# Kernel optimization log

Measured on AMD Instinct MI355X. Metric: run time of the kernel, lower is better.

## Reference

```python
import jax, jax.numpy as jnp
import numpy as np

DT = 0.01
OMEGA_MAX = 100.0


def setup_inputs() -> dict:
    key = jax.random.key(0)
    ks = jax.random.split(key, 7)
    B, T, D, M = 4, 4096, 1024, 64
    N = 2 * M
    u = jax.random.normal(ks[0], (B, T, D), dtype=jnp.float32)
    W_omega = jax.random.normal(ks[1], (M, D), dtype=jnp.float32) * 0.02
    b_omega = jnp.ones((M,), dtype=jnp.float32)
    W_zeta = jax.random.normal(ks[2], (M, D), dtype=jnp.float32) * 0.02
    b_zeta = jnp.zeros((M,), dtype=jnp.float32)
    W_B = jax.random.normal(ks[3], (N, D), dtype=jnp.float32) * (0.1 / np.sqrt(D))
    b_B = jnp.zeros((N,), dtype=jnp.float32)
    C = jax.random.normal(ks[4], (D, N), dtype=jnp.float32) * 0.01
    D_mat = jax.random.normal(ks[5], (D, D), dtype=jnp.float32) * 0.01
    return dict(u=u, W_omega=W_omega, b_omega=b_omega, W_zeta=W_zeta,
                b_zeta=b_zeta, W_B=W_B, b_B=b_B, C=C, D_mat=D_mat)


def reference(u, W_omega, b_omega, W_zeta, b_zeta, W_B, b_B, C, D_mat):
    B, T, D = u.shape
    M = W_omega.shape[0]
    # Hoist all per-step linear projections into batched GEMMs (same math).
    omega = jax.nn.softplus(jnp.einsum('btd,md->btm', u, W_omega) + b_omega)
    omega = jnp.clip(omega, 1e-4, OMEGA_MAX)                      # (B,T,M)
    zeta = jax.nn.sigmoid(jnp.einsum('btd,md->btm', u, W_zeta) + b_zeta)
    A = omega * omega                                             # (B,T,M)
    S = 1.0 / (1.0 + (DT * DT) * A)                               # (B,T,M)
    d = 1.0 - zeta                                                # (B,T,M)
    F = jnp.einsum('btd,nd->btn', u, W_B) + b_B                   # (B,T,2M)

    def step(x, inp):
        A_t, S_t, d_t, F_t = inp                                  # (B,M)x3, (B,2M)
        z = x[:, :M]
        y = x[:, M:]
        z_new = d_t * (S_t * z - DT * A_t * S_t * y)
        y_new = d_t * (DT * S_t * z + S_t * y)
        x_new = jnp.concatenate([z_new, y_new], axis=-1) + F_t
        return x_new, x_new

    x0 = jnp.zeros((B, 2 * M), dtype=u.dtype)
    tm = lambda a: jnp.swapaxes(a, 0, 1)  # to time-major for scan
    _, xs = jax.lax.scan(step, x0, (tm(A), tm(S), tm(d), tm(F)))
    xs = jnp.swapaxes(xs, 0, 1)                                   # (B,T,2M)
    # Output projection: y_t = x_t C^T + u_t D^T
    y = jnp.einsum('btn,dn->btd', xs, C) + jnp.einsum('bte,de->btd', u, D_mat)
    return y
```

## Files before the change

### kernel.cpp

```cpp
#include <hip/hip_runtime.h>
#include <hip/hip_bf16.h>
#include <math.h>

#define DTC 0.01f

typedef __attribute__((ext_vector_type(8))) short short8;
typedef __attribute__((ext_vector_type(4))) float f32x4;
typedef unsigned short bf16raw;

__device__ __forceinline__ bf16raw f2bf(float f){
  union { unsigned u; float f; } v; v.f = f;
  unsigned r = v.u + 0x7FFF + ((v.u >> 16) & 1u);
  return (bf16raw)(r >> 16);
}

__device__ __forceinline__ short8 ld8f(const float* __restrict__ p){
  float4 a = *(const float4*)p;
  float4 b = *(const float4*)(p + 4);
  short8 r;
  r[0] = (short)f2bf(a.x); r[1] = (short)f2bf(a.y);
  r[2] = (short)f2bf(a.z); r[3] = (short)f2bf(a.w);
  r[4] = (short)f2bf(b.x); r[5] = (short)f2bf(b.y);
  r[6] = (short)f2bf(b.z); r[7] = (short)f2bf(b.w);
  return r;
}

template<int ITERS>
__device__ __forceinline__ void stage_async(const bf16raw* __restrict__ src, long ld,
                                            long row0, int k0, bf16raw* lds,
                                            int wave, int lane){
  int kchunk = (lane & 3) ^ ((lane >> 3) & 3);
#pragma unroll
  for (int i = 0; i < ITERS; ++i){
    int r0 = (wave*ITERS + i) * 16;
    long row = row0 + r0 + (lane >> 2);
    const bf16raw* gp = src + row*ld + k0 + kchunk*8;
    bf16raw* lp = lds + r0*32;
    __builtin_amdgcn_global_load_lds((const __attribute__((address_space(1))) void*)gp,
                                     (__attribute__((address_space(3))) void*)lp,
                                     16, 0, 0);
  }
}

template<int MI, int NI>
__device__ __forceinline__ void mma_tile(const bf16raw* Alds, const bf16raw* Blds,
                                         f32x4 acc[MI][NI], int wm, int wn, int quad, int t16){
  short8 af[MI], bfr[NI];
  int sw = (quad ^ ((t16 >> 1) & 3)) * 8;
#pragma unroll
  for (int mi = 0; mi < MI; ++mi)
    af[mi] = *(const short8*)(Alds + (wm*(MI*16) + mi*16 + t16)*32 + sw);
#pragma unroll
  for (int ni = 0; ni < NI; ++ni)
    bfr[ni] = *(const short8*)(Blds + (wn*(NI*16) + ni*16 + t16)*32 + sw);
#pragma unroll
  for (int mi = 0; mi < MI; ++mi)
#pragma unroll
    for (int ni = 0; ni < NI; ++ni)
      acc[mi][ni] = __builtin_amdgcn_mfma_f32_16x16x32_bf16(af[mi], bfr[ni], acc[mi][ni], 0, 0, 0);
}

extern "C" __global__ void k_prep(const float* __restrict__ u,
    const float* __restrict__ Wom, const float* __restrict__ Wze,
    const float* __restrict__ WB, const float* __restrict__ Cm,
    const float* __restrict__ Dm, bf16raw* __restrict__ u_bf,
    bf16raw* __restrict__ Wcat, bf16raw* __restrict__ C_bf,
    bf16raw* __restrict__ Dm_bf){
  long g = (long)blockIdx.x * 256 + threadIdx.x;
  const float* src; bf16raw* dst; long o;
  if      (g < 2097152){ src = u;   dst = u_bf;          o = g; }
  else if (g < 2105344){ src = Wom; dst = Wcat;          o = g - 2097152; }
  else if (g < 2113536){ src = Wze; dst = Wcat + 65536;  o = g - 2105344; }
  else if (g < 2129920){ src = WB;  dst = Wcat + 131072; o = g - 2113536; }
  else if (g < 2146304){ src = Cm;  dst = C_bf;          o = g - 2129920; }
  else                 { src = Dm;  dst = Dm_bf;         o = g - 2146304; }
  *(short8*)(dst + o*8) = ld8f(src + o*8);
}

extern "C" __global__ __launch_bounds__(256, 4) void k_gemm_p(
    const bf16raw* __restrict__ u_bf, const bf16raw* __restrict__ Wcat,
    float* __restrict__ P){
  __shared__ __align__(16) bf16raw Alds[3*64*32];
  __shared__ __align__(16) bf16raw Blds[3*64*32];
  int tid = threadIdx.x, wave = tid >> 6, lane = tid & 63;
  int quad = lane >> 4, t16 = lane & 15;
  int wm = wave >> 1, wn = wave & 1;
  int id  = blockIdx.y * gridDim.x + blockIdx.x;
  int sid = (id & 7) * 128 + (id >> 3);
  long row0 = (long)(sid >> 2) * 64;
  int  col0 = (sid & 3) * 64;
  f32x4 acc[2][2] = {};

  auto stage = [&](int kt, int buf){
    stage_async<1>(u_bf, 1024, row0, kt*32, Alds + buf*(64*32), wave, lane);
    stage_async<1>(Wcat, 1024, col0, kt*32, Blds + buf*(64*32), wave, lane);
  };

  stage(0, 0);
  stage(1, 1);
  int rd = 0;
  for (int s = 0; s < 30; ++s){
    asm volatile("s_waitcnt vmcnt(2)" ::: "memory");
    __builtin_amdgcn_s_barrier();
    __builtin_amdgcn_sched_barrier(0);
    int st = rd >= 1 ? rd - 1 : 2;
    stage(s + 2, st);
    __builtin_amdgcn_s_setprio(1);
    mma_tile<2,2>(Alds + rd*(64*32), Blds + rd*(64*32), acc, wm, wn, quad, t16);
    __builtin_amdgcn_s_setprio(0);
    rd = rd < 2 ? rd + 1 : 0;
  }
  asm volatile("s_waitcnt vmcnt(2)" ::: "memory");
  __builtin_amdgcn_s_barrier();
  __builtin_amdgcn_sched_barrier(0);
  mma_tile<2,2>(Alds + 0*(64*32), Blds + 0*(64*32), acc, wm, wn, quad, t16);
  asm volatile("s_waitcnt vmcnt(0)" ::: "memory");
  __builtin_amdgcn_s_barrier();
  __builtin_amdgcn_sched_barrier(0);
  mma_tile<2,2>(Alds + 1*(64*32), Blds + 1*(64*32), acc, wm, wn, quad, t16);
#pragma unroll
  for (int mi = 0; mi < 2; ++mi)
#pragma unroll
    for (int ni = 0; ni < 2; ++ni)
#pragma unroll
      for (int r = 0; r < 4; ++r){
        long grow = row0 + wm*32 + mi*16 + quad*4 + r;
        int  gcol = col0 + wn*32 + ni*16 + t16;
        P[grow*256 + gcol] = acc[mi][ni][r];
      }
}

extern "C" __global__ __launch_bounds__(256, 3) void k_gemm_out(
    const bf16raw* __restrict__ Xs, const bf16raw* __restrict__ u_bf,
    const bf16raw* __restrict__ C_bf, const bf16raw* __restrict__ Dm_bf,
    float* __restrict__ out){
  __shared__ __align__(16) bf16raw Alds[3*128*32];
  __shared__ __align__(16) bf16raw Blds[3*128*32];
  int tid = threadIdx.x, wave = tid >> 6, lane = tid & 63;
  int quad = lane >> 4, t16 = lane & 15;
  int wm = wave >> 1, wn = wave & 1;
  int id  = blockIdx.y * gridDim.x + blockIdx.x;
  int sid = (id & 7) * 128 + (id >> 3);
  long row0 = (long)(sid >> 3) * 128;
  int  col0 = (sid & 7) * 128;
  f32x4 acc[4][4] = {};

  auto stage = [&](int s, int buf){
    if (s < 4){
      stage_async<2>(Xs,   128, row0, s*32, Alds + buf*(128*32), wave, lane);
      stage_async<2>(C_bf, 128, col0, s*32, Blds + buf*(128*32), wave, lane);
    } else {
      stage_async<2>(u_bf,  1024, row0, (s-4)*32, Alds + buf*(128*32), wave, lane);
      stage_async<2>(Dm_bf, 1024, col0, (s-4)*32, Blds + buf*(128*32), wave, lane);
    }
  };

  stage(0, 0);
  stage(1, 1);
  int rd = 0;
  for (int s = 0; s < 34; ++s){
    asm volatile("s_waitcnt vmcnt(4)" ::: "memory");
    __builtin_amdgcn_s_barrier();
    __builtin_amdgcn_sched_barrier(0);
    int st = rd >= 1 ? rd - 1 : 2;
    stage(s + 2, st);
    __builtin_amdgcn_s_setprio(1);
    mma_tile<4,4>(Alds + rd*(128*32), Blds + rd*(128*32), acc, wm, wn, quad, t16);
    __builtin_amdgcn_s_setprio(0);
    rd = rd < 2 ? rd + 1 : 0;
  }
  asm volatile("s_waitcnt vmcnt(4)" ::: "memory");
  __builtin_amdgcn_s_barrier();
  __builtin_amdgcn_sched_barrier(0);
  mma_tile<4,4>(Alds + 1*(128*32), Blds + 1*(128*32), acc, wm, wn, quad, t16);
  asm volatile("s_waitcnt vmcnt(0)" ::: "memory");
  __builtin_amdgcn_s_barrier();
  __builtin_amdgcn_sched_barrier(0);
  mma_tile<4,4>(Alds + 2*(128*32), Blds + 2*(128*32), acc, wm, wn, quad, t16);
#pragma unroll
  for (int mi = 0; mi < 4; ++mi)
#pragma unroll
    for (int ni = 0; ni < 4; ++ni)
#pragma unroll
      for (int r = 0; r < 4; ++r){
        long grow = row0 + wm*64 + mi*16 + quad*4 + r;
        int  gcol = col0 + wn*64 + ni*16 + t16;
        out[grow*1024 + gcol] = acc[mi][ni][r];
      }
}

extern "C" __global__ __launch_bounds__(256) void k_scanA(
    const float* __restrict__ P, const float* __restrict__ b_om,
    const float* __restrict__ b_ze, const float* __restrict__ b_B,
    float4* __restrict__ CM, float2* __restrict__ CV){
  int tid = threadIdx.x, c = blockIdx.x;
  int b = tid >> 6, m = tid & 63;
  float bo = b_om[m], bz = b_ze[m], bb0 = b_B[m], bb1 = b_B[64 + m];
  const float* row = P + ((size_t)b*4096 + c*16) * 256;
  float m00=1.f, m01=0.f, m10=0.f, m11=0.f, vz=0.f, vy=0.f;
#pragma unroll 4
  for (int t = 0; t < 16; ++t){
    const float* r = row + t*256;
    float wo = r[m]       + bo;
    float wz = r[64 + m]  + bz;
    float fz = r[128 + m] + bb0;
    float fy = r[192 + m] + bb1;
    float sp = (wo > 20.f) ? wo : log1pf(expf(wo));
    float omega = fminf(fmaxf(sp, 1e-4f), 100.f);
    float A = omega * omega;
    float S = 1.f / (1.f + DTC*DTC*A);
    float zeta = 1.f / (1.f + expf(-wz));
    float p = (1.f - zeta) * S;
    float q = p * DTC * A;
    float nvz = p*vz - q*vy + fz;
    float nvy = DTC*p*vz + p*vy + fy;
    vz = nvz; vy = nvy;
    float n00 = p*m00 - q*m10;
    float n01 = p*m01 - q*m11;
    float n10 = DTC*p*m00 + p*m10;
    float n11 = DTC*p*m01 + p*m11;
    m00=n00; m01=n01; m10=n10; m11=n11;
  }
  CM[c*256 + tid] = make_float4(m00, m01, m10, m11);
  CV[c*256 + tid] = make_float2(vz, vy);
}

extern "C" __global__ __launch_bounds__(256) void k_scanC(
    const float* __restrict__ P, const float* __restrict__ b_om,
    const float* __restrict__ b_ze, const float* __restrict__ b_B,
    const float4* __restrict__ CM, const float2* __restrict__ CV,
    bf16raw* __restrict__ Xs){
  int tid = threadIdx.x, c = blockIdx.x;
  int b = tid >> 6, m = tid & 63;
  float xz = 0.f, xy = 0.f;
#pragma unroll 4
  for (int j = 0; j < c; ++j){
    float4 Mv = CM[j*256 + tid];
    float2 Vv = CV[j*256 + tid];
    float nz = Mv.x*xz + Mv.y*xy + Vv.x;
    float ny = Mv.z*xz + Mv.w*xy + Vv.y;
    xz = nz; xy = ny;
  }
  float bo = b_om[m], bz = b_ze[m], bb0 = b_B[m], bb1 = b_B[64 + m];
  const float* row = P + ((size_t)b*4096 + c*16) * 256;
  bf16raw* xp = Xs + ((size_t)b*4096 + c*16) * 128 + m;
#pragma unroll 4
  for (int t = 0; t < 16; ++t){
    const float* r = row + t*256;
    float wo = r[m]       + bo;
    float wz = r[64 + m]  + bz;
    float fz = r[128 + m] + bb0;
    float fy = r[192 + m] + bb1;
    float sp = (wo > 20.f) ? wo : log1pf(expf(wo));
    float omega = fminf(fmaxf(sp, 1e-4f), 100.f);
    float A = omega * omega;
    float S = 1.f / (1.f + DTC*DTC*A);
    float zeta = 1.f / (1.f + expf(-wz));
    float p = (1.f - zeta) * S;
    float q = p * DTC * A;
    float nz = p*xz - q*xy + fz;
    float ny = DTC*p*xz + p*xy + fy;
    xz = nz; xy = ny;
    xp[t*128]      = f2bf(xz);
    xp[t*128 + 64] = f2bf(xy);
  }
}

extern "C" void kernel_launch(void* const* d_in, const int* in_sizes, int n_in,
                              void* d_out, int out_size, void* d_ws, size_t ws_size,
                              hipStream_t stream){
  const float* u   = (const float*)d_in[0];
  const float* Wom = (const float*)d_in[1];
  const float* bom = (const float*)d_in[2];
  const float* Wze = (const float*)d_in[3];
  const float* bze = (const float*)d_in[4];
  const float* WB  = (const float*)d_in[5];
  const float* bB  = (const float*)d_in[6];
  const float* Cm  = (const float*)d_in[7];
  const float* Dm  = (const float*)d_in[8];
  float* out = (float*)d_out;

  char* ws = (char*)d_ws;
  size_t off = 0;
  bf16raw* u_bf  = (bf16raw*)(ws + off); off += (size_t)16777216*2;
  bf16raw* Wcat  = (bf16raw*)(ws + off); off += (size_t)262144*2;
  bf16raw* C_bf  = (bf16raw*)(ws + off); off += (size_t)131072*2;
  bf16raw* Dm_bf = (bf16raw*)(ws + off); off += (size_t)1048576*2;
  float*   P     = (float*)  (ws + off); off += (size_t)16384*256*4;
  bf16raw* Xs    = (bf16raw*)(ws + off); off += (size_t)16384*128*2;
  float4*  CMw   = (float4*) (ws + off); off += (size_t)256*256*16;
  float2*  CVw   = (float2*) (ws + off); off += (size_t)256*256*8;

  k_prep    <<<8896, 256, 0, stream>>>(u, Wom, Wze, WB, Cm, Dm, u_bf, Wcat, C_bf, Dm_bf);
  k_gemm_p  <<<dim3(4, 256), 256, 0, stream>>>(u_bf, Wcat, P);
  k_scanA   <<<256, 256, 0, stream>>>(P, bom, bze, bB, CMw, CVw);
  k_scanC   <<<256, 256, 0, stream>>>(P, bom, bze, bB, CMw, CVw, Xs);
  k_gemm_out<<<dim3(8, 128), 256, 0, stream>>>(Xs, u_bf, C_bf, Dm_bf, out);
}
```

Measured before the change: 240.4 us.

## Parallelize chunk-carry scan and widen output GEMM tile to 128x256

```diff
diff --git a/kernel.cpp b/kernel.cpp
--- a/kernel.cpp
+++ b/kernel.cpp
@@ -130,28 +130,28 @@
       }
 }
 
-extern "C" __global__ __launch_bounds__(256, 3) void k_gemm_out(
+extern "C" __global__ __launch_bounds__(256, 2) void k_gemm_out(
     const bf16raw* __restrict__ Xs, const bf16raw* __restrict__ u_bf,
     const bf16raw* __restrict__ C_bf, const bf16raw* __restrict__ Dm_bf,
     float* __restrict__ out){
   __shared__ __align__(16) bf16raw Alds[3*128*32];
-  __shared__ __align__(16) bf16raw Blds[3*128*32];
+  __shared__ __align__(16) bf16raw Blds[3*256*32];
   int tid = threadIdx.x, wave = tid >> 6, lane = tid & 63;
   int quad = lane >> 4, t16 = lane & 15;
   int wm = wave >> 1, wn = wave & 1;
   int id  = blockIdx.y * gridDim.x + blockIdx.x;
-  int sid = (id & 7) * 128 + (id >> 3);
-  long row0 = (long)(sid >> 3) * 128;
-  int  col0 = (sid & 7) * 128;
-  f32x4 acc[4][4] = {};
+  int sid = (id & 7) * 64 + (id >> 3);
+  long row0 = (long)(sid >> 2) * 128;
+  int  col0 = (sid & 3) * 256;
+  f32x4 acc[4][8] = {};
 
   auto stage = [&](int s, int buf){
     if (s < 4){
       stage_async<2>(Xs,   128, row0, s*32, Alds + buf*(128*32), wave, lane);
-      stage_async<2>(C_bf, 128, col0, s*32, Blds + buf*(128*32), wave, lane);
+      stage_async<4>(C_bf, 128, col0, s*32, Blds + buf*(256*32), wave, lane);
     } else {
       stage_async<2>(u_bf,  1024, row0, (s-4)*32, Alds + buf*(128*32), wave, lane);
-      stage_async<2>(Dm_bf, 1024, col0, (s-4)*32, Blds + buf*(128*32), wave, lane);
+      stage_async<4>(Dm_bf, 1024, col0, (s-4)*32, Blds + buf*(256*32), wave, lane);
     }
   };
 
@@ -159,32 +159,32 @@
   stage(1, 1);
   int rd = 0;
   for (int s = 0; s < 34; ++s){
-    asm volatile("s_waitcnt vmcnt(4)" ::: "memory");
+    asm volatile("s_waitcnt vmcnt(6)" ::: "memory");
     __builtin_amdgcn_s_barrier();
     __builtin_amdgcn_sched_barrier(0);
     int st = rd >= 1 ? rd - 1 : 2;
     stage(s + 2, st);
     __builtin_amdgcn_s_setprio(1);
-    mma_tile<4,4>(Alds + rd*(128*32), Blds + rd*(128*32), acc, wm, wn, quad, t16);
+    mma_tile<4,8>(Alds + rd*(128*32), Blds + rd*(256*32), acc, wm, wn, quad, t16);
     __builtin_amdgcn_s_setprio(0);
     rd = rd < 2 ? rd + 1 : 0;
   }
-  asm volatile("s_waitcnt vmcnt(4)" ::: "memory");
+  asm volatile("s_waitcnt vmcnt(6)" ::: "memory");
   __builtin_amdgcn_s_barrier();
   __builtin_amdgcn_sched_barrier(0);
-  mma_tile<4,4>(Alds + 1*(128*32), Blds + 1*(128*32), acc, wm, wn, quad, t16);
+  mma_tile<4,8>(Alds + 1*(128*32), Blds + 1*(256*32), acc, wm, wn, quad, t16);
   asm volatile("s_waitcnt vmcnt(0)" ::: "memory");
   __builtin_amdgcn_s_barrier();
   __builtin_amdgcn_sched_barrier(0);
-  mma_tile<4,4>(Alds + 2*(128*32), Blds + 2*(128*32), acc, wm, wn, quad, t16);
+  mma_tile<4,8>(Alds + 2*(128*32), Blds + 2*(256*32), acc, wm, wn, quad, t16);
 #pragma unroll
   for (int mi = 0; mi < 4; ++mi)
 #pragma unroll
-    for (int ni = 0; ni < 4; ++ni)
+    for (int ni = 0; ni < 8; ++ni)
 #pragma unroll
       for (int r = 0; r < 4; ++r){
         long grow = row0 + wm*64 + mi*16 + quad*4 + r;
-        int  gcol = col0 + wn*64 + ni*16 + t16;
+        int  gcol = col0 + wn*128 + ni*16 + t16;
         out[grow*1024 + gcol] = acc[mi][ni][r];
       }
 }
@@ -225,22 +225,45 @@
   CV[c*256 + tid] = make_float2(vz, vy);
 }
 
+extern "C" __global__ __launch_bounds__(256) void k_scanB(
+    const float4* __restrict__ CM, const float2* __restrict__ CV,
+    float2* __restrict__ XIn){
+  __shared__ float sm[6][256];
+  int s = blockIdx.x;
+  int c = threadIdx.x;
+  float4 Mv = CM[(size_t)c*256 + s];
+  float2 Vv = CV[(size_t)c*256 + s];
+  float m00=Mv.x, m01=Mv.y, m10=Mv.z, m11=Mv.w, vz=Vv.x, vy=Vv.y;
+#pragma unroll
+  for (int off = 1; off < 256; off <<= 1){
+    sm[0][c]=m00; sm[1][c]=m01; sm[2][c]=m10; sm[3][c]=m11; sm[4][c]=vz; sm[5][c]=vy;
+    __syncthreads();
+    if (c >= off){
+      int p = c - off;
+      float e00=sm[0][p], e01=sm[1][p], e10=sm[2][p], e11=sm[3][p];
+      float evz=sm[4][p], evy=sm[5][p];
+      float n00 = m00*e00 + m01*e10;
+      float n01 = m00*e01 + m01*e11;
+      float n10 = m10*e00 + m11*e10;
+      float n11 = m10*e01 + m11*e11;
+      float nvz = m00*evz + m01*evy + vz;
+      float nvy = m10*evz + m11*evy + vy;
+      m00=n00; m01=n01; m10=n10; m11=n11; vz=nvz; vy=nvy;
+    }
+    __syncthreads();
+  }
+  if (c < 255) XIn[(size_t)(c+1)*256 + s] = make_float2(vz, vy);
+  if (c == 0)  XIn[s] = make_float2(0.f, 0.f);
+}
+
 extern "C" __global__ __launch_bounds__(256) void k_scanC(
     const float* __restrict__ P, const float* __restrict__ b_om,
     const float* __restrict__ b_ze, const float* __restrict__ b_B,
-    const float4* __restrict__ CM, const float2* __restrict__ CV,
-    bf16raw* __restrict__ Xs){
+    const float2* __restrict__ XIn, bf16raw* __restrict__ Xs){
   int tid = threadIdx.x, c = blockIdx.x;
   int b = tid >> 6, m = tid & 63;
-  float xz = 0.f, xy = 0.f;
-#pragma unroll 4
-  for (int j = 0; j < c; ++j){
-    float4 Mv = CM[j*256 + tid];
-    float2 Vv = CV[j*256 + tid];
-    float nz = Mv.x*xz + Mv.y*xy + Vv.x;
-    float ny = Mv.z*xz + Mv.w*xy + Vv.y;
-    xz = nz; xy = ny;
-  }
+  float2 x0 = XIn[(size_t)c*256 + tid];
+  float xz = x0.x, xy = x0.y;
   float bo = b_om[m], bz = b_ze[m], bb0 = b_B[m], bb1 = b_B[64 + m];
   const float* row = P + ((size_t)b*4096 + c*16) * 256;
   bf16raw* xp = Xs + ((size_t)b*4096 + c*16) * 128 + m;
@@ -290,10 +313,12 @@
   bf16raw* Xs    = (bf16raw*)(ws + off); off += (size_t)16384*128*2;
   float4*  CMw   = (float4*) (ws + off); off += (size_t)256*256*16;
   float2*  CVw   = (float2*) (ws + off); off += (size_t)256*256*8;
+  float2*  XIn   = (float2*) (ws + off); off += (size_t)256*256*8;
 
   k_prep    <<<8896, 256, 0, stream>>>(u, Wom, Wze, WB, Cm, Dm, u_bf, Wcat, C_bf, Dm_bf);
   k_gemm_p  <<<dim3(4, 256), 256, 0, stream>>>(u_bf, Wcat, P);
   k_scanA   <<<256, 256, 0, stream>>>(P, bom, bze, bB, CMw, CVw);
-  k_scanC   <<<256, 256, 0, stream>>>(P, bom, bze, bB, CMw, CVw, Xs);
-  k_gemm_out<<<dim3(8, 128), 256, 0, stream>>>(Xs, u_bf, C_bf, Dm_bf, out);
-}
+  k_scanB   <<<256, 256, 0, stream>>>(CMw, CVw, XIn);
+  k_scanC   <<<256, 256, 0, stream>>>(P, bom, bze, bB, XIn, Xs);
+  k_gemm_out<<<dim3(4, 128), 256, 0, stream>>>(Xs, u_bf, C_bf, Dm_bf, out);
+}
```

After: 214.3 us. -10.8%, faster.
